# Kernel optimization log

Measured on AMD Instinct MI355X. Metric: run time of the kernel, lower is better.

## Reference

```python
import jax, jax.numpy as jnp
import numpy as np
from jax import lax

K = 3          # kernel_size
PAD = 1        # replication padding
EPS = 1e-5     # BatchNorm2d eps


def setup_inputs() -> dict:
    key = jax.random.key(0)
    k1, k2, k3, k4 = jax.random.split(key, 4)
    B, Cin, O, H, W = 16, 64, 128, 32, 32
    x = jax.random.normal(k1, (B, Cin + 5, H, W), dtype=jnp.float32)
    conv_w = jax.random.normal(k2, (O, Cin, K, K), dtype=jnp.float32) * 0.05
    conv_b = jax.random.normal(k3, (O,), dtype=jnp.float32) * 0.05
    shapes_kernel = jax.random.normal(k4, (O, 5, K * K), dtype=jnp.float32)
    return {"x": x, "conv_w": conv_w, "conv_b": conv_b, "shapes_kernel": shapes_kernel}


def _bn_noaffine(y):
    # BatchNorm2d(affine=False) in training mode: batch stats over (N, H, W)
    m = jnp.mean(y, axis=(0, 2, 3), keepdims=True)
    v = jnp.mean((y - m) ** 2, axis=(0, 2, 3), keepdims=True)
    return (y - m) / jnp.sqrt(v + EPS)


def reference(x, conv_w, conv_b, shapes_kernel):
    B = x.shape[0]
    # replication padding
    xp = jnp.pad(x, ((0, 0), (0, 0), (PAD, PAD), (PAD, PAD)), mode="edge")
    feat, shp = xp[:, :-5], xp[:, -5:]

    # conv branch: VALID conv on feature channels -> (B, O, H, W)
    conv_out = lax.conv_general_dilated(
        feat, conv_w, window_strides=(1, 1), padding="VALID",
        dimension_numbers=("NCHW", "OIHW", "NCHW"),
    ) + conv_b[None, :, None, None]
    H, W = conv_out.shape[2], conv_out.shape[3]
    NW = H * W

    # unfold(x_padded[:, -5:], K): patches (B, 5, K*K, NW), channel-major like torch
    patches = jnp.stack(
        [shp[:, :, i:i + H, j:j + W] for i in range(K) for j in range(K)], axis=2
    ).reshape(B, 5, K * K, NW)

    # center the first two (x,y coordinate) channels on the window center
    c = K * K // 2
    centered_xy = patches[:, :2] - patches[:, :2, c:c + 1]
    windows = jnp.concatenate([centered_xy, patches[:, 2:]], axis=1)  # (B,5,KK,NW)

    # L1 distance against learned shape kernel: (B, O, NW)
    delta = windows[:, None] - shapes_kernel[None, :, :, :, None]  # (B,O,5,KK,NW)
    shape_difference = jnp.sum(jnp.abs(delta), axis=(2, 3))

    # fold with (1,1) kernel == reshape to image
    sdw = shape_difference.reshape(B, -1, H, W)
    muxed = jax.nn.relu(_bn_noaffine(sdw))

    conv_bn = _bn_noaffine(conv_out)
    attended = jax.nn.relu(conv_bn - muxed)

    # pass the 5 shape channels through unchanged
    return jnp.concatenate([attended, x[:, -5:]], axis=1)
```

## Files before the change

kernel.cpp:

```cpp
#include <hip/hip_runtime.h>

typedef __attribute__((ext_vector_type(8))) __bf16 bf16x8;
typedef __attribute__((ext_vector_type(4))) float f32x4;

#define NB 16
#define CIN 64
#define CT 69
#define NO 128
#define HWSZ 1024
#define OUTC 133

__device__ __forceinline__ unsigned pack_bf16(float a, float b) {
    unsigned ua = __float_as_uint(a);
    ua += 0x7fffu + ((ua >> 16) & 1u);
    unsigned ub = __float_as_uint(b);
    ub += 0x7fffu + ((ub >> 16) & 1u);
    return (ua >> 16) | (ub & 0xffff0000u);
}

__device__ __forceinline__ float bf16rt(float a) {
    unsigned u = __float_as_uint(a);
    u += 0x7fffu + ((u >> 16) & 1u);
    return __uint_as_float(u & 0xffff0000u);
}

__device__ __forceinline__ void gload16(const void* g, void* l) {
    __builtin_amdgcn_global_load_lds(
        (const __attribute__((address_space(1))) unsigned int*)g,
        (__attribute__((address_space(3))) unsigned int*)l, 16, 0, 0);
}

__global__ __launch_bounds__(512) void prep_sdw_kernel(
    const float* __restrict__ x, const float* __restrict__ cw,
    const float* __restrict__ sk, unsigned* __restrict__ xT,
    unsigned* __restrict__ wT, unsigned short* __restrict__ sdwb,
    float* __restrict__ sdwpart, float* __restrict__ out)
{
    int bl = blockIdx.x;
    int tid = threadIdx.x;

    if (bl < 512) {
        int chg = bl >> 5;
        int slice = bl & 31;
        int pix = slice * 512 + tid;
        int b = pix >> 10;
        int hw = pix & 1023;
        int h = hw >> 5, w = hw & 31;

        float win[45];
#pragma unroll
        for (int ch = 0; ch < 5; ++ch) {
            const float* xb = x + (((size_t)b * CT + CIN + ch) << 10);
#pragma unroll
            for (int ki = 0; ki < 3; ++ki) {
                int rr = h + ki - 1;
                rr = rr < 0 ? 0 : (rr > 31 ? 31 : rr);
                const float* rp = xb + (rr << 5);
#pragma unroll
                for (int kj = 0; kj < 3; ++kj) {
                    int cc = w + kj - 1;
                    cc = cc < 0 ? 0 : (cc > 31 ? 31 : cc);
                    win[ch * 9 + ki * 3 + kj] = rp[cc];
                }
            }
        }
#pragma unroll
        for (int ch = 0; ch < 2; ++ch) {
            float c = win[ch * 9 + 4];
#pragma unroll
            for (int k = 0; k < 9; ++k) win[ch * 9 + k] -= c;
        }
#pragma unroll
        for (int q = 0; q < 45; ++q) asm volatile("" : "+v"(win[q]));

        int wid = tid >> 6;
        int wslot = slice * 8 + wid;
        for (int j = 0; j < 8; ++j) {
            int ch = chg * 8 + j;
            const float* kk = sk + (size_t)ch * 45;
            float s = 0.f;
#pragma unroll
            for (int q = 0; q < 45; ++q) s += fabsf(win[q] - kk[q]);
            unsigned u = __float_as_uint(s);
            u += 0x7fffu + ((u >> 16) & 1u);
            sdwb[(((size_t)b * NO + ch) << 10) + hw] = (unsigned short)(u >> 16);
            float sr = __uint_as_float(u & 0xffff0000u);
            float ps = sr, ps2 = sr * sr;
#pragma unroll
            for (int off = 32; off; off >>= 1) {
                ps  += __shfl_xor(ps, off);
                ps2 += __shfl_xor(ps2, off);
            }
            if ((tid & 63) == 0) {
                sdwpart[((size_t)ch * 256 + wslot) * 2]     = ps;
                sdwpart[((size_t)ch * 256 + wslot) * 2 + 1] = ps2;
            }
        }
    } else if (bl < 768) {
        int v = (bl - 512) * 512 + tid;
        int blk2 = v >> 8;
        int t2 = v & 255;
        int b = blk2 >> 5, h = blk2 & 31;
        int w = t2 & 31, cp0 = t2 >> 5;
        const float* xr = x + (((size_t)b * CT) << 10) + h * 32 + w;
        unsigned* dst = xT + (size_t)blk2 * 1024 + w * 32;
        int sw = (w & 7) << 2;
#pragma unroll
        for (int r = 0; r < 4; ++r) {
            int cp = cp0 + r * 8;
            dst[cp ^ sw] = pack_bf16(xr[(size_t)(2 * cp) << 10],
                                     xr[(size_t)(2 * cp + 1) << 10]);
        }
    } else if (bl < 776) {
        int tg = (bl - 768) * 512 + tid;
        int o = tg >> 5, cp = tg & 31;
        int sw = (o & 7) << 2;
#pragma unroll
        for (int tap = 0; tap < 9; ++tap) {
            float v0 = cw[((size_t)o * CIN + 2 * cp) * 9 + tap];
            float v1 = cw[((size_t)o * CIN + 2 * cp + 1) * 9 + tap];
            wT[tap * 4096 + o * 32 + (cp ^ sw)] = pack_bf16(v0, v1);
        }
    } else {
        int idx = (bl - 776) * 512 + tid;
        int q = idx & 255;
        int c = (idx >> 8) % 5;
        int b = (idx >> 8) / 5;
        ((float4*)out)[((size_t)b * OUTC + NO + c) * 256 + q] =
            ((const float4*)x)[((size_t)b * CT + CIN + c) * 256 + q];
    }
}

__global__ __launch_bounds__(512) void conv_mfma_kernel(
    const char* __restrict__ xT, const char* __restrict__ wT,
    unsigned short* __restrict__ convb, float* __restrict__ convpart)
{
    __shared__ __align__(16) char smem[65536];
    char* Xs = smem;
    char* Wb0 = smem + 16384;
    char* Wb1 = smem + 32768;
    char* Wb2 = smem + 49152;

    int bid = blockIdx.x;
    int b = bid >> 4;
    int h0 = (bid & 15) * 2;

    int tid = threadIdx.x;
    int lane = tid & 63;
    int wid = tid >> 6;
    int lo = lane & 15, g = lane >> 4;
    int ks = wid >> 2;
    int mg = (wid >> 1) & 1;
    int ng = wid & 1;

#pragma unroll
    for (int q = 0; q < 2; ++q) {
        int ch = wid * 2 + q;
        int s = ch >> 2;
        int srch = h0 - 1 + s; srch = srch < 0 ? 0 : (srch > 31 ? 31 : srch);
        gload16(xT + ((size_t)(b * 32 + srch)) * 4096 + (ch & 3) * 1024 + lane * 16,
                Xs + ch * 1024);
    }
#pragma unroll
    for (int q = 0; q < 2; ++q) {
        int ch = wid * 2 + q;
        gload16(wT + ch * 1024 + lane * 16, Wb0 + ch * 1024);
    }
#pragma unroll
    for (int q = 0; q < 2; ++q) {
        int ch = wid * 2 + q;
        gload16(wT + 16384 + ch * 1024 + lane * 16, Wb1 + ch * 1024);
    }

    int acol[2][3];
#pragma unroll
    for (int i = 0; i < 2; ++i)
#pragma unroll
        for (int kj = 0; kj < 3; ++kj) {
            int cin = i * 16 + lo + kj - 1;
            cin = cin < 0 ? 0 : (cin > 31 ? 31 : cin);
            acol[i][kj] = cin * 128 + ((ks * 64 + g * 16) ^ ((cin & 7) << 4));
        }
    int boff[4];
#pragma unroll
    for (int n = 0; n < 4; ++n) {
        int o = ng * 64 + n * 16 + lo;
        boff[n] = o * 128 + ((ks * 64 + g * 16) ^ ((o & 7) << 4));
    }

    f32x4 acc[2][4];
#pragma unroll
    for (int i = 0; i < 2; ++i)
#pragma unroll
        for (int n = 0; n < 4; ++n) acc[i][n] = (f32x4){0.f, 0.f, 0.f, 0.f};

#pragma unroll
    for (int tap = 0; tap < 9; ++tap) {
        int ki = tap / 3, kj = tap % 3;
        if (tap == 8) asm volatile("s_waitcnt vmcnt(0)" ::: "memory");
        else          asm volatile("s_waitcnt vmcnt(2)" ::: "memory");
        __builtin_amdgcn_sched_barrier(0);
        __builtin_amdgcn_s_barrier();
        __builtin_amdgcn_sched_barrier(0);
        if (tap + 2 < 9) {
            char* wn = ((tap + 2) % 3 == 0) ? Wb0 : ((tap + 2) % 3 == 1) ? Wb1 : Wb2;
#pragma unroll
            for (int q = 0; q < 2; ++q) {
                int ch = wid * 2 + q;
                gload16(wT + (size_t)(tap + 2) * 16384 + ch * 1024 + lane * 16,
                        wn + ch * 1024);
            }
        }
        const char* wc = (tap % 3 == 0) ? Wb0 : (tap % 3 == 1) ? Wb1 : Wb2;
        bf16x8 a0 = *(const bf16x8*)(Xs + (mg + ki) * 4096 + acol[0][kj]);
        bf16x8 a1 = *(const bf16x8*)(Xs + (mg + ki) * 4096 + acol[1][kj]);
#pragma unroll
        for (int n = 0; n < 4; ++n) {
            bf16x8 bv = *(const bf16x8*)(wc + boff[n]);
            acc[0][n] = __builtin_amdgcn_mfma_f32_16x16x32_bf16(a0, bv, acc[0][n], 0, 0, 0);
            acc[1][n] = __builtin_amdgcn_mfma_f32_16x16x32_bf16(a1, bv, acc[1][n], 0, 0, 0);
        }
    }
    __syncthreads();

    float* T = (float*)smem;
    if (ks == 1) {
#pragma unroll
        for (int i = 0; i < 2; ++i)
#pragma unroll
            for (int n = 0; n < 4; ++n)
#pragma unroll
                for (int r = 0; r < 4; ++r) {
                    int pixel = (mg * 2 + i) * 16 + g * 4 + r;
                    int o = ng * 64 + n * 16 + lo;
                    T[pixel * 129 + o] = acc[i][n][r];
                }
    }
    __syncthreads();
    if (ks == 0) {
#pragma unroll
        for (int i = 0; i < 2; ++i)
#pragma unroll
            for (int n = 0; n < 4; ++n)
#pragma unroll
                for (int r = 0; r < 4; ++r) {
                    int pixel = (mg * 2 + i) * 16 + g * 4 + r;
                    int o = ng * 64 + n * 16 + lo;
                    T[pixel * 129 + o] += acc[i][n][r];
                }
    }
    __syncthreads();
    unsigned short* cbase = convb + (((size_t)b * NO) << 10) + h0 * 32;
#pragma unroll
    for (int r = 0; r < 4; ++r) {
        int o = r * 32 + (tid >> 4);
        int pq = tid & 15;
        float4 v;
        v.x = T[(pq * 4 + 0) * 129 + o];
        v.y = T[(pq * 4 + 1) * 129 + o];
        v.z = T[(pq * 4 + 2) * 129 + o];
        v.w = T[(pq * 4 + 3) * 129 + o];
        uint2 pk;
        pk.x = pack_bf16(v.x, v.y);
        pk.y = pack_bf16(v.z, v.w);
        *(uint2*)(cbase + ((size_t)o << 10) + pq * 4) = pk;
        float rx = bf16rt(v.x), ry = bf16rt(v.y);
        float rz = bf16rt(v.z), rw = bf16rt(v.w);
        float s  = rx + ry + rz + rw;
        float s2 = rx * rx + ry * ry + rz * rz + rw * rw;
#pragma unroll
        for (int off = 1; off < 16; off <<= 1) {
            s  += __shfl_xor(s, off);
            s2 += __shfl_xor(s2, off);
        }
        if (pq == 0) {
            convpart[((size_t)o * 256 + bid) * 2]     = s;
            convpart[((size_t)o * 256 + bid) * 2 + 1] = s2;
        }
    }
}

__global__ __launch_bounds__(512) void final_kernel(
    const unsigned short* __restrict__ sdwb,
    const unsigned short* __restrict__ convb,
    const float* __restrict__ convpart, const float* __restrict__ sdwpart,
    float* __restrict__ out)
{
    __shared__ float st[32];
    int bl = blockIdx.x;
    int tid = threadIdx.x;
    int b = bl >> 4;
    int o0 = (bl & 15) * 8;

    int lane = tid & 63;
    int wid = tid >> 6;
    {
        int ch = o0 + wid;
        double cs = 0.0, cs2 = 0.0, ss = 0.0, ss2 = 0.0;
#pragma unroll
        for (int q = 0; q < 4; ++q) {
            int slot = lane + q * 64;
            const float* cp = convpart + ((size_t)ch * 256 + slot) * 2;
            cs  += cp[0]; cs2 += cp[1];
            const float* sp = sdwpart + ((size_t)ch * 256 + slot) * 2;
            ss  += sp[0]; ss2 += sp[1];
        }
#pragma unroll
        for (int off = 32; off; off >>= 1) {
            cs  += __shfl_down(cs, off);
            cs2 += __shfl_down(cs2, off);
            ss  += __shfl_down(ss, off);
            ss2 += __shfl_down(ss2, off);
        }
        if (lane == 0) {
            double n = 16384.0;
            double cm = cs / n, cv = cs2 / n - cm * cm;
            double sm = ss / n, sv = ss2 / n - sm * sm;
            st[wid * 4]     = (float)cm;
            st[wid * 4 + 1] = (float)(1.0 / sqrt(cv + 1e-5));
            st[wid * 4 + 2] = (float)sm;
            st[wid * 4 + 3] = (float)(1.0 / sqrt(sv + 1e-5));
        }
    }
    __syncthreads();

#pragma unroll
    for (int k = 0; k < 2; ++k) {
        int ql = tid + k * 512;
        int pl = ql >> 7;
        int g8 = ql & 127;
        int o = o0 + pl;
        size_t ebase = (((size_t)b * NO + o) << 10) + g8 * 8;
        uint4 cu = *(const uint4*)(convb + ebase);
        uint4 su = *(const uint4*)(sdwb + ebase);
        float cm = st[pl * 4], cis = st[pl * 4 + 1];
        float sm = st[pl * 4 + 2], sis = st[pl * 4 + 3];
        float4 r0, r1;
        float cv, sv, mu, v;
        unsigned uc, us;
        uc = cu.x; us = su.x;
        cv = __uint_as_float(uc << 16); sv = __uint_as_float(us << 16);
        mu = (sv - sm) * sis; mu = mu > 0.f ? mu : 0.f;
        v = (cv - cm) * cis - mu; r0.x = v > 0.f ? v : 0.f;
        cv = __uint_as_float(uc & 0xffff0000u); sv = __uint_as_float(us & 0xffff0000u);
        mu = (sv - sm) * sis; mu = mu > 0.f ? mu : 0.f;
        v = (cv - cm) * cis - mu; r0.y = v > 0.f ? v : 0.f;
        uc = cu.y; us = su.y;
        cv = __uint_as_float(uc << 16); sv = __uint_as_float(us << 16);
        mu = (sv - sm) * sis; mu = mu > 0.f ? mu : 0.f;
        v = (cv - cm) * cis - mu; r0.z = v > 0.f ? v : 0.f;
        cv = __uint_as_float(uc & 0xffff0000u); sv = __uint_as_float(us & 0xffff0000u);
        mu = (sv - sm) * sis; mu = mu > 0.f ? mu : 0.f;
        v = (cv - cm) * cis - mu; r0.w = v > 0.f ? v : 0.f;
        uc = cu.z; us = su.z;
        cv = __uint_as_float(uc << 16); sv = __uint_as_float(us << 16);
        mu = (sv - sm) * sis; mu = mu > 0.f ? mu : 0.f;
        v = (cv - cm) * cis - mu; r1.x = v > 0.f ? v : 0.f;
        cv = __uint_as_float(uc & 0xffff0000u); sv = __uint_as_float(us & 0xffff0000u);
        mu = (sv - sm) * sis; mu = mu > 0.f ? mu : 0.f;
        v = (cv - cm) * cis - mu; r1.y = v > 0.f ? v : 0.f;
        uc = cu.w; us = su.w;
        cv = __uint_as_float(uc << 16); sv = __uint_as_float(us << 16);
        mu = (sv - sm) * sis; mu = mu > 0.f ? mu : 0.f;
        v = (cv - cm) * cis - mu; r1.z = v > 0.f ? v : 0.f;
        cv = __uint_as_float(uc & 0xffff0000u); sv = __uint_as_float(us & 0xffff0000u);
        mu = (sv - sm) * sis; mu = mu > 0.f ? mu : 0.f;
        v = (cv - cm) * cis - mu; r1.w = v > 0.f ? v : 0.f;
        float* ob = out + (((size_t)b * OUTC + o) << 10) + g8 * 8;
        *(float4*)ob = r0;
        *(float4*)(ob + 4) = r1;
    }
}

extern "C" void kernel_launch(void* const* d_in, const int* in_sizes, int n_in,
                              void* d_out, int out_size, void* d_ws, size_t ws_size,
                              hipStream_t stream)
{
    const float* x  = (const float*)d_in[0];
    const float* cw = (const float*)d_in[1];
    const float* sk = (const float*)d_in[3];
    float* out = (float*)d_out;

    unsigned short* sdwb  = (unsigned short*)d_ws;
    unsigned short* convb = (unsigned short*)((char*)d_ws + 0x400000);
    unsigned* xT       = (unsigned*)((char*)d_ws + 0x810000);
    unsigned* wT       = (unsigned*)((char*)d_ws + 0xA10000);
    float*    convpart = (float*)((char*)d_ws + 0xA40000);
    float*    sdwpart  = (float*)((char*)d_ws + 0xA80000);

    prep_sdw_kernel<<<816, 512, 0, stream>>>(x, cw, sk, xT, wT, sdwb, sdwpart, out);
    conv_mfma_kernel<<<256, 512, 0, stream>>>((const char*)xT, (const char*)wT,
                                              convb, convpart);
    final_kernel   <<<256, 512, 0, stream>>>(sdwb, convb, convpart, sdwpart, out);
}
```

Baseline: 30.79 us.

## Move shape-difference computation into conv kernel launch to overlap with MFMA conv

The shape-difference (sdw) work moves out of the prep kernel and into extra blocks of the conv kernel, so the L1-distance computation runs alongside the MFMA convolution instead of before it. The prep kernel now only does the transposes, weight packing and passthrough copy, which shortens the critical path before the conv starts. The risk is that sdw blocks inherit the conv kernel's 64KB LDS allocation and register budget, which limits occupancy. The noinline call may also add overhead.

```diff
diff --git a/kernel.cpp b/kernel.cpp
--- a/kernel.cpp
+++ b/kernel.cpp
@@ -30,74 +30,16 @@
         (__attribute__((address_space(3))) unsigned int*)l, 16, 0, 0);
 }
 
-__global__ __launch_bounds__(512) void prep_sdw_kernel(
+__global__ __launch_bounds__(512) void prep_kernel(
     const float* __restrict__ x, const float* __restrict__ cw,
-    const float* __restrict__ sk, unsigned* __restrict__ xT,
-    unsigned* __restrict__ wT, unsigned short* __restrict__ sdwb,
-    float* __restrict__ sdwpart, float* __restrict__ out)
+    unsigned* __restrict__ xT, unsigned* __restrict__ wT,
+    float* __restrict__ out)
 {
     int bl = blockIdx.x;
     int tid = threadIdx.x;
 
-    if (bl < 512) {
-        int chg = bl >> 5;
-        int slice = bl & 31;
-        int pix = slice * 512 + tid;
-        int b = pix >> 10;
-        int hw = pix & 1023;
-        int h = hw >> 5, w = hw & 31;
-
-        float win[45];
-#pragma unroll
-        for (int ch = 0; ch < 5; ++ch) {
-            const float* xb = x + (((size_t)b * CT + CIN + ch) << 10);
-#pragma unroll
-            for (int ki = 0; ki < 3; ++ki) {
-                int rr = h + ki - 1;
-                rr = rr < 0 ? 0 : (rr > 31 ? 31 : rr);
-                const float* rp = xb + (rr << 5);
-#pragma unroll
-                for (int kj = 0; kj < 3; ++kj) {
-                    int cc = w + kj - 1;
-                    cc = cc < 0 ? 0 : (cc > 31 ? 31 : cc);
-                    win[ch * 9 + ki * 3 + kj] = rp[cc];
-                }
-            }
-        }
-#pragma unroll
-        for (int ch = 0; ch < 2; ++ch) {
-            float c = win[ch * 9 + 4];
-#pragma unroll
-            for (int k = 0; k < 9; ++k) win[ch * 9 + k] -= c;
-        }
-#pragma unroll
-        for (int q = 0; q < 45; ++q) asm volatile("" : "+v"(win[q]));
-
-        int wid = tid >> 6;
-        int wslot = slice * 8 + wid;
-        for (int j = 0; j < 8; ++j) {
-            int ch = chg * 8 + j;
-            const float* kk = sk + (size_t)ch * 45;
-            float s = 0.f;
-#pragma unroll
-            for (int q = 0; q < 45; ++q) s += fabsf(win[q] - kk[q]);
-            unsigned u = __float_as_uint(s);
-            u += 0x7fffu + ((u >> 16) & 1u);
-            sdwb[(((size_t)b * NO + ch) << 10) + hw] = (unsigned short)(u >> 16);
-            float sr = __uint_as_float(u & 0xffff0000u);
-            float ps = sr, ps2 = sr * sr;
-#pragma unroll
-            for (int off = 32; off; off >>= 1) {
-                ps  += __shfl_xor(ps, off);
-                ps2 += __shfl_xor(ps2, off);
-            }
-            if ((tid & 63) == 0) {
-                sdwpart[((size_t)ch * 256 + wslot) * 2]     = ps;
-                sdwpart[((size_t)ch * 256 + wslot) * 2 + 1] = ps2;
-            }
-        }
-    } else if (bl < 768) {
-        int v = (bl - 512) * 512 + tid;
+    if (bl < 256) {
+        int v = bl * 512 + tid;
         int blk2 = v >> 8;
         int t2 = v & 255;
         int b = blk2 >> 5, h = blk2 & 31;
@@ -111,8 +53,8 @@
             dst[cp ^ sw] = pack_bf16(xr[(size_t)(2 * cp) << 10],
                                      xr[(size_t)(2 * cp + 1) << 10]);
         }
-    } else if (bl < 776) {
-        int tg = (bl - 768) * 512 + tid;
+    } else if (bl < 264) {
+        int tg = (bl - 256) * 512 + tid;
         int o = tg >> 5, cp = tg & 31;
         int sw = (o & 7) << 2;
 #pragma unroll
@@ -122,7 +64,7 @@
             wT[tap * 4096 + o * 32 + (cp ^ sw)] = pack_bf16(v0, v1);
         }
     } else {
-        int idx = (bl - 776) * 512 + tid;
+        int idx = (bl - 264) * 512 + tid;
         int q = idx & 255;
         int c = (idx >> 8) % 5;
         int b = (idx >> 8) / 5;
@@ -131,11 +73,83 @@
     }
 }
 
-__global__ __launch_bounds__(512) void conv_mfma_kernel(
+__device__ __noinline__ void sdw_body(
+    const float* __restrict__ x, const float* __restrict__ sk,
+    unsigned short* __restrict__ sdwb, float* __restrict__ sdwpart,
+    int sbl, int tid)
+{
+    int chg = sbl >> 5;
+    int slice = sbl & 31;
+    int pix = slice * 512 + tid;
+    int b = pix >> 10;
+    int hw = pix & 1023;
+    int h = hw >> 5, w = hw & 31;
+
+    float win[45];
+#pragma unroll
+    for (int ch = 0; ch < 5; ++ch) {
+        const float* xb = x + (((size_t)b * CT + CIN + ch) << 10);
+#pragma unroll
+        for (int ki = 0; ki < 3; ++ki) {
+            int rr = h + ki - 1;
+            rr = rr < 0 ? 0 : (rr > 31 ? 31 : rr);
+            const float* rp = xb + (rr << 5);
+#pragma unroll
+            for (int kj = 0; kj < 3; ++kj) {
+                int cc = w + kj - 1;
+                cc = cc < 0 ? 0 : (cc > 31 ? 31 : cc);
+                win[ch * 9 + ki * 3 + kj] = rp[cc];
+            }
+        }
+    }
+#pragma unroll
+    for (int ch = 0; ch < 2; ++ch) {
+        float c = win[ch * 9 + 4];
+#pragma unroll
+        for (int k = 0; k < 9; ++k) win[ch * 9 + k] -= c;
+    }
+#pragma unroll
+    for (int q = 0; q < 45; ++q) asm volatile("" : "+v"(win[q]));
+
+    int wid = tid >> 6;
+    int wslot = slice * 8 + wid;
+    for (int j = 0; j < 8; ++j) {
+        int ch = chg * 8 + j;
+        const float* kk = sk + (size_t)ch * 45;
+        float s = 0.f;
+#pragma unroll
+        for (int q = 0; q < 45; ++q) s += fabsf(win[q] - kk[q]);
+        unsigned u = __float_as_uint(s);
+        u += 0x7fffu + ((u >> 16) & 1u);
+        sdwb[(((size_t)b * NO + ch) << 10) + hw] = (unsigned short)(u >> 16);
+        float sr = __uint_as_float(u & 0xffff0000u);
+        float ps = sr, ps2 = sr * sr;
+#pragma unroll
+        for (int off = 32; off; off >>= 1) {
+            ps  += __shfl_xor(ps, off);
+            ps2 += __shfl_xor(ps2, off);
+        }
+        if ((tid & 63) == 0) {
+            sdwpart[((size_t)ch * 256 + wslot) * 2]     = ps;
+            sdwpart[((size_t)ch * 256 + wslot) * 2 + 1] = ps2;
+        }
+    }
+}
+
+__global__ __launch_bounds__(512) void convsdw_kernel(
     const char* __restrict__ xT, const char* __restrict__ wT,
-    unsigned short* __restrict__ convb, float* __restrict__ convpart)
+    const float* __restrict__ x, const float* __restrict__ sk,
+    unsigned short* __restrict__ convb, float* __restrict__ convpart,
+    unsigned short* __restrict__ sdwb, float* __restrict__ sdwpart)
 {
     __shared__ __align__(16) char smem[65536];
+    int tid = threadIdx.x;
+
+    if (blockIdx.x >= 256) {
+        sdw_body(x, sk, sdwb, sdwpart, blockIdx.x - 256, tid);
+        return;
+    }
+
     char* Xs = smem;
     char* Wb0 = smem + 16384;
     char* Wb1 = smem + 32768;
@@ -145,7 +159,6 @@
     int b = bid >> 4;
     int h0 = (bid & 15) * 2;
 
-    int tid = threadIdx.x;
     int lane = tid & 63;
     int wid = tid >> 6;
     int lo = lane & 15, g = lane >> 4;
@@ -388,8 +401,8 @@
     float*    convpart = (float*)((char*)d_ws + 0xA40000);
     float*    sdwpart  = (float*)((char*)d_ws + 0xA80000);
 
-    prep_sdw_kernel<<<816, 512, 0, stream>>>(x, cw, sk, xT, wT, sdwb, sdwpart, out);
-    conv_mfma_kernel<<<256, 512, 0, stream>>>((const char*)xT, (const char*)wT,
-                                              convb, convpart);
-    final_kernel   <<<256, 512, 0, stream>>>(sdwb, convb, convpart, sdwpart, out);
-}
+    prep_kernel   <<<304, 512, 0, stream>>>(x, cw, xT, wT, out);
+    convsdw_kernel<<<768, 512, 0, stream>>>((const char*)xT, (const char*)wT,
+                                            x, sk, convb, convpart, sdwb, sdwpart);
+    final_kernel  <<<256, 512, 0, stream>>>(sdwb, convb, convpart, sdwpart, out);
+}
```

Measured after the change: 49.93 us. +62.2%, slower.
